# Performance work log

Hardware: AMD Instinct MI355X
Metric: run time of the kernel (lower is better)

The kernel has to match this reference:

```python
import jax, jax.numpy as jnp
import numpy as np

B, S, D = 4, 2048, 1024
H, K = 16, 64
EPS = 1e-3  # Keras LayerNormalization default epsilon


def setup_inputs() -> dict:
    key = jax.random.key(0)
    ks = jax.random.split(key, 11)
    s = 0.02
    return {
        "x":  jax.random.normal(ks[0], (B, S, D), jnp.float32),
        "Wq": jax.random.normal(ks[1], (D, H, K), jnp.float32) * s,
        "bq": jnp.zeros((H, K), jnp.float32),
        "Wk": jax.random.normal(ks[2], (D, H, K), jnp.float32) * s,
        "bk": jnp.zeros((H, K), jnp.float32),
        "Wv": jax.random.normal(ks[3], (D, H, K), jnp.float32) * s,
        "bv": jnp.zeros((H, K), jnp.float32),
        "Wo": jax.random.normal(ks[4], (H, K, D), jnp.float32) * s,
        "bo": jnp.zeros((D,), jnp.float32),
        "gamma": jnp.ones((D,), jnp.float32),
        "beta":  jnp.zeros((D,), jnp.float32),
    }


def reference(x, Wq, bq, Wk, bk, Wv, bv, Wo, bo, gamma, beta):
    # QKV projections (Keras MHA einsum form): [B,S,D] -> [B,S,H,K]
    q = jnp.einsum("bsd,dhk->bshk", x, Wq) + bq
    k = jnp.einsum("bsd,dhk->bshk", x, Wk) + bk
    v = jnp.einsum("bsd,dhk->bshk", x, Wv) + bv
    scale = 1.0 / jnp.sqrt(jnp.asarray(K, x.dtype))
    scores = jnp.einsum("bqhk,bshk->bhqs", q, k) * scale  # [B,H,S,S]
    attn = jax.nn.softmax(scores, axis=-1)
    ctx = jnp.einsum("bhqs,bshk->bqhk", attn, v)           # [B,S,H,K]
    attn_out = jnp.einsum("bqhk,hkd->bqd", ctx, Wo) + bo   # [B,S,D]
    # residual + LayerNorm (over last axis)
    y = x + attn_out
    mu = jnp.mean(y, axis=-1, keepdims=True)
    var = jnp.mean(jnp.square(y - mu), axis=-1, keepdims=True)
    return (y - mu) * jax.lax.rsqrt(var + EPS) * gamma + beta
```

## Files before the change

### kernel.cpp

```cpp
#include <hip/hip_runtime.h>

typedef float f32x4 __attribute__((ext_vector_type(4)));
typedef float f32x16 __attribute__((ext_vector_type(16)));
typedef __bf16 bf16x8 __attribute__((ext_vector_type(8)));
typedef __bf16 bf16x4 __attribute__((ext_vector_type(4)));
typedef __bf16 bf16x2 __attribute__((ext_vector_type(2)));
typedef unsigned short us4 __attribute__((ext_vector_type(4)));

#define DEV __device__ __forceinline__

DEV unsigned short f2bf(float f) {
  union { float f; unsigned int u; } v; v.f = f;
  unsigned int u = v.u;
  return (unsigned short)((u + 0x7FFFu + ((u >> 16) & 1u)) >> 16);
}

typedef const __attribute__((address_space(1))) void* gvp;
typedef __attribute__((address_space(3))) void* lvp;

DEV void gll16(const void* g, void* l) {
  __builtin_amdgcn_global_load_lds((gvp)g, (lvp)l, 16, 0, 0);
}

DEV float fexp2(float x) { return __builtin_amdgcn_exp2f(x); }

DEV void plswap(unsigned& a, unsigned& b) {
  asm("v_permlane32_swap_b32 %0, %1" : "+v"(a), "+v"(b));
}
DEV float xhalf_sum(float v) {
  union { float f; unsigned u; } a, b;
  a.f = v; b.f = v;
  plswap(a.u, b.u);
  return a.f + b.f;
}

__global__ void k_convert(const float* __restrict__ in, unsigned short* __restrict__ out, int n4) {
  int i = blockIdx.x * blockDim.x + threadIdx.x;
  if (i < n4) {
    float4 v = ((const float4*)in)[i];
    us4 o = { f2bf(v.x), f2bf(v.y), f2bf(v.z), f2bf(v.w) };
    ((us4*)out)[i] = o;
  }
}

__global__ void k_transpose4(const float* __restrict__ w0, const float* __restrict__ w1,
                             const float* __restrict__ w2, const float* __restrict__ w3,
                             unsigned short* __restrict__ o0, unsigned short* __restrict__ o1,
                             unsigned short* __restrict__ o2, unsigned short* __restrict__ o3) {
  const float* in = (blockIdx.z == 0) ? w0 : (blockIdx.z == 1) ? w1 : (blockIdx.z == 2) ? w2 : w3;
  unsigned short* out = (blockIdx.z == 0) ? o0 : (blockIdx.z == 1) ? o1 : (blockIdx.z == 2) ? o2 : o3;
  __shared__ float tile[32][33];
  const int bx = blockIdx.x * 32, by = blockIdx.y * 32;
  const int tx = threadIdx.x, ty = threadIdx.y;
#pragma unroll
  for (int r = 0; r < 4; ++r)
    tile[ty + r * 8][tx] = in[(size_t)(by + ty + r * 8) * 1024 + bx + tx];
  __syncthreads();
#pragma unroll
  for (int r = 0; r < 4; ++r)
    out[(size_t)(bx + ty + r * 8) * 1024 + by + tx] = f2bf(tile[tx][ty + r * 8]);
}

__global__ void k_gemm_qkv(const unsigned short* __restrict__ xb,
                           const unsigned short* __restrict__ wqt,
                           const unsigned short* __restrict__ wkt,
                           const unsigned short* __restrict__ wvt,
                           const float* __restrict__ bq, const float* __restrict__ bk,
                           const float* __restrict__ bv,
                           unsigned short* __restrict__ qb, unsigned short* __restrict__ kb,
                           unsigned short* __restrict__ vtb) {
  __shared__ unsigned short SM[2][128 * 64];
  unsigned short* As = SM[0];
  unsigned short* Bs = SM[1];
  const int tid = threadIdx.x;
  const int lane = tid & 63;
  const int wave = tid >> 6;
  const int l15 = lane & 15;
  const int lq  = lane >> 4;
  const int wm = wave >> 1, wn = wave & 1;
  const int z = blockIdx.z;

  const unsigned short* A;
  const unsigned short* Bt;
  int mbase, nbase;
  if (z == 2) { A = wvt; Bt = xb; mbase = blockIdx.y * 128; nbase = blockIdx.x * 128; }
  else        { A = xb; Bt = z ? wkt : wqt; mbase = blockIdx.x * 128; nbase = blockIdx.y * 128; }

  f32x4 acc[4][4] = {};

  for (int kt = 0; kt < 1024; kt += 64) {
    __syncthreads();
#pragma unroll
    for (int c = 0; c < 4; ++c) {
      int e = (c * 256 + tid) * 8;
      int row = e >> 6;
      int o2 = (e * 2) ^ ((row & 7) << 4);
      int col = (o2 >> 1) & 63;
      gll16(A + (size_t)(mbase + row) * 1024 + kt + col,
            As + (c * 256 + (tid & ~63)) * 8);
      gll16(Bt + (size_t)(nbase + row) * 1024 + kt + col,
            Bs + (c * 256 + (tid & ~63)) * 8);
    }
    __syncthreads();
#pragma unroll
    for (int ks = 0; ks < 2; ++ks) {
      bf16x8 af[4], bfv[4];
#pragma unroll
      for (int i = 0; i < 4; ++i) {
        int row = wm * 64 + i * 16 + l15;
        int off = row * 128 + ((((ks << 2) | lq) ^ (row & 7)) << 4);
        af[i] = *(const bf16x8*)((const char*)As + off);
      }
#pragma unroll
      for (int j = 0; j < 4; ++j) {
        int row = wn * 64 + j * 16 + l15;
        int off = row * 128 + ((((ks << 2) | lq) ^ (row & 7)) << 4);
        bfv[j] = *(const bf16x8*)((const char*)Bs + off);
      }
#pragma unroll
      for (int i = 0; i < 4; ++i)
#pragma unroll
        for (int j = 0; j < 4; ++j)
          acc[i][j] = __builtin_amdgcn_mfma_f32_16x16x32_bf16(bfv[j], af[i], acc[i][j], 0, 0, 0);
    }
  }

  const float scale = (z == 0) ? 0.18033688011112042f : 1.0f;
  const float* bias = (z == 0) ? bq : (z == 1) ? bk : bv;
  unsigned short* outp = (z == 0) ? qb : (z == 1) ? kb : vtb;

  float4 bj[4];
  if (z < 2) {
#pragma unroll
    for (int j = 0; j < 4; ++j)
      bj[j] = *(const float4*)&bias[nbase + wn * 64 + j * 16 + lq * 4];
  }

  __syncthreads();
  char* T = (char*)SM;
#pragma unroll
  for (int i = 0; i < 4; ++i) {
    const int miL = wm * 64 + i * 16 + l15;
    const int sw = (miL & 7) << 4;
    const float bm = (z == 2) ? bias[mbase + miL] : 0.f;
#pragma unroll
    for (int j = 0; j < 4; ++j) {
      const int nj2 = (wn * 64 + j * 16 + lq * 4) * 2;
      bf16x4 p;
#pragma unroll
      for (int r = 0; r < 4; ++r) {
        float v = acc[i][j][r];
        v = (z < 2) ? (v + ((const float*)&bj[j])[r]) * scale : (v + bm);
        p[r] = (__bf16)v;
      }
      *(bf16x4*)(T + miL * 256 + (nj2 ^ sw)) = p;
    }
  }
  __syncthreads();

#pragma unroll
  for (int c = 0; c < 8; ++c) {
    const int lin = c * 256 + tid;
    const int row = lin >> 4;
    const int s16 = lin & 15;
    bf16x8 vv = *(const bf16x8*)(T + row * 256 + ((s16 * 16) ^ ((row & 7) << 4)));
    const int mi = mbase + row;
    const int nj = nbase + s16 * 8;
    size_t gaddr;
    if (z < 2) {
      gaddr = (((size_t)((mi >> 11) * 16 + (nj >> 6)) * 2048 + (mi & 2047)) << 6) + (nj & 63);
    } else {
      gaddr = ((size_t)(((nj >> 11) * 16 + (mi >> 6)) * 64 + (mi & 63))) * 2048 + (nj & 2047);
    }
    *(bf16x8*)(outp + gaddr) = vv;
  }
}

__global__ void k_gemm_out(const unsigned short* __restrict__ A,
                           const unsigned short* __restrict__ Bt,
                           const float* __restrict__ bias,
                           float* __restrict__ outp,
                           const float* __restrict__ xres) {
  __shared__ unsigned short As[128 * 64];
  __shared__ unsigned short Bs[128 * 64];
  const int tid = threadIdx.x;
  const int lane = tid & 63;
  const int wave = tid >> 6;
  const int l15 = lane & 15;
  const int lq  = lane >> 4;
  const int wm = wave >> 1, wn = wave & 1;
  const int mbase = blockIdx.x * 128;
  const int nbase = blockIdx.y * 128;

  f32x4 acc[4][4] = {};

  for (int kt = 0; kt < 1024; kt += 64) {
    __syncthreads();
#pragma unroll
    for (int c = 0; c < 4; ++c) {
      int e = (c * 256 + tid) * 8;
      int row = e >> 6;
      int o2 = (e * 2) ^ ((row & 7) << 4);
      int col = (o2 >> 1) & 63;
      gll16(A + (size_t)(mbase + row) * 1024 + kt + col,
            As + (c * 256 + (tid & ~63)) * 8);
      gll16(Bt + (size_t)(nbase + row) * 1024 + kt + col,
            Bs + (c * 256 + (tid & ~63)) * 8);
    }
    __syncthreads();
#pragma unroll
    for (int ks = 0; ks < 2; ++ks) {
      bf16x8 af[4], bfv[4];
#pragma unroll
      for (int i = 0; i < 4; ++i) {
        int row = wm * 64 + i * 16 + l15;
        int off = row * 128 + ((((ks << 2) | lq) ^ (row & 7)) << 4);
        af[i] = *(const bf16x8*)((const char*)As + off);
      }
#pragma unroll
      for (int j = 0; j < 4; ++j) {
        int row = wn * 64 + j * 16 + l15;
        int off = row * 128 + ((((ks << 2) | lq) ^ (row & 7)) << 4);
        bfv[j] = *(const bf16x8*)((const char*)Bs + off);
      }
#pragma unroll
      for (int i = 0; i < 4; ++i)
#pragma unroll
        for (int j = 0; j < 4; ++j)
          acc[i][j] = __builtin_amdgcn_mfma_f32_16x16x32_bf16(af[i], bfv[j], acc[i][j], 0, 0, 0);
    }
  }

#pragma unroll
  for (int i = 0; i < 4; ++i)
#pragma unroll
    for (int j = 0; j < 4; ++j)
#pragma unroll
      for (int r = 0; r < 4; ++r) {
        int mi = mbase + wm * 64 + i * 16 + lq * 4 + r;
        int nj = nbase + wn * 64 + j * 16 + l15;
        size_t idx = (size_t)mi * 1024 + nj;
        outp[idx] = acc[i][j][r] + bias[nj] + xres[idx];
      }
}

__global__ __launch_bounds__(256, 4) void k_attn(const unsigned short* __restrict__ q,
                       const unsigned short* __restrict__ k,
                       const unsigned short* __restrict__ vt,
                       unsigned short* __restrict__ ctx) {
  __shared__ unsigned short KV[2][2][64 * 64];

  const int tid = threadIdx.x;
  const int lane = tid & 63;
  const int wave = tid >> 6;
  const int l31 = lane & 31;
  const int l5 = lane >> 5;

  const int bid = blockIdx.x;
  const int swz = (bid & 7) * 128 + (bid >> 3);
  const int bh = swz >> 4;
  const int qtile = swz & 15;
  const int qbase = qtile * 128;
  const size_t sl = (size_t)bh << 17;

  const int qrow = qbase + wave * 32 + l31;
  bf16x8 qreg[4];
#pragma unroll
  for (int ds = 0; ds < 4; ++ds)
    qreg[ds] = *(const bf16x8*)(q + sl + (size_t)qrow * 64 + ds * 16 + l5 * 8);

#define STAGE_KV(BUF, TT) do {                                                 \
    const int kvb_ = (TT) * 64;                                                \
    _Pragma("unroll")                                                          \
    for (int c = 0; c < 2; ++c) {                                              \
      int e = (c * 256 + tid) * 8;                                             \
      int row_ = e >> 6;                                                       \
      int o2 = (e * 2) ^ ((row_ & 7) << 4);                                    \
      int col_ = (o2 >> 1) & 63;                                               \
      gll16(k + sl + (size_t)(kvb_ + row_) * 64 + col_,                        \
            KV[BUF][0] + (c * 256 + (tid & ~63)) * 8);                         \
      gll16(vt + sl + (size_t)row_ * 2048 + kvb_ + col_,                       \
            KV[BUF][1] + (c * 256 + (tid & ~63)) * 8);                         \
    }                                                                          \
  } while (0)

  STAGE_KV(0, 0);
  __syncthreads();

  f32x16 acc0 = {}, acc1 = {};
  float lrow = 0.f;

  for (int t = 0; t < 32; ++t) {
    const int cur = t & 1;
    if (t < 31) STAGE_KV(cur ^ 1, t + 1);

    const char* Ksc = (const char*)KV[cur][0];
    const char* Vtc = (const char*)KV[cur][1];

    bf16x8 kf0[4], kf1[4];
#pragma unroll
    for (int ds = 0; ds < 4; ++ds) {
      int r0 = l31, r1 = 32 + l31;
      kf0[ds] = *(const bf16x8*)(Ksc + r0 * 128 + ((ds * 32 + l5 * 16) ^ ((r0 & 7) << 4)));
      kf1[ds] = *(const bf16x8*)(Ksc + r1 * 128 + ((ds * 32 + l5 * 16) ^ ((r1 & 7) << 4)));
    }
    f32x16 s0 = {}, s1 = {};
    __builtin_amdgcn_s_setprio(1);
#pragma unroll
    for (int ds = 0; ds < 4; ++ds)
      s0 = __builtin_amdgcn_mfma_f32_32x32x16_bf16(kf0[ds], qreg[ds], s0, 0, 0, 0);
#pragma unroll
    for (int ds = 0; ds < 4; ++ds)
      s1 = __builtin_amdgcn_mfma_f32_32x32x16_bf16(kf1[ds], qreg[ds], s1, 0, 0, 0);
    __builtin_amdgcn_s_setprio(0);
    __builtin_amdgcn_sched_barrier(0);

    unsigned pk0[8], pk1[8];
    float r0s = 0.f, r1s = 0.f, r2s = 0.f, r3s = 0.f;
#pragma unroll
    for (int m = 0; m < 8; ++m) {
      float a0 = fexp2(s0[2 * m]), a1 = fexp2(s0[2 * m + 1]);
      float b0 = fexp2(s1[2 * m]), b1 = fexp2(s1[2 * m + 1]);
      r0s += a0; r1s += a1; r2s += b0; r3s += b1;
      union { bf16x2 v; unsigned u; } ua, ub;
      ua.v = bf16x2{ (__bf16)a0, (__bf16)a1 };
      ub.v = bf16x2{ (__bf16)b0, (__bf16)b1 };
      pk0[m] = ua.u; pk1[m] = ub.u;
    }
    lrow += (r0s + r1s) + (r2s + r3s);
    __builtin_amdgcn_sched_barrier(0);

    bf16x8 av0[4], av1[4];
#pragma unroll
    for (int kvg = 0; kvg < 4; ++kvg) {
      int r0 = l31, r1 = 32 + l31;
      av0[kvg] = *(const bf16x8*)(Vtc + r0 * 128 + ((kvg * 32 + l5 * 16) ^ ((r0 & 7) << 4)));
      av1[kvg] = *(const bf16x8*)(Vtc + r1 * 128 + ((kvg * 32 + l5 * 16) ^ ((r1 & 7) << 4)));
    }
#pragma unroll
    for (int kvh = 0; kvh < 2; ++kvh) {
      unsigned* pk = kvh ? pk1 : pk0;
#pragma unroll
      for (int g = 0; g < 2; ++g) {
        unsigned a0_ = pk[4 * g],     b0_ = pk[4 * g + 2];
        unsigned a1_ = pk[4 * g + 1], b1_ = pk[4 * g + 3];
        plswap(a0_, b0_);
        plswap(a1_, b1_);
        union { unsigned u[4]; bf16x8 v; } pf;
        pf.u[0] = a0_; pf.u[1] = a1_; pf.u[2] = b0_; pf.u[3] = b1_;
        const int kvg = 2 * kvh + g;
        __builtin_amdgcn_s_setprio(1);
        acc0 = __builtin_amdgcn_mfma_f32_32x32x16_bf16(av0[kvg], pf.v, acc0, 0, 0, 0);
        acc1 = __builtin_amdgcn_mfma_f32_32x32x16_bf16(av1[kvg], pf.v, acc1, 0, 0, 0);
        __builtin_amdgcn_s_setprio(0);
      }
    }

    __syncthreads();
  }

  const float inv = 1.f / xhalf_sum(lrow);

  unsigned short* TR = (unsigned short*)KV;
  const int qloc = wave * 32 + l31;
  const int swq = (qloc & 7) << 4;
#pragma unroll
  for (int dh = 0; dh < 2; ++dh) {
    const f32x16& ac = dh ? acc1 : acc0;
#pragma unroll
    for (int g3 = 0; g3 < 4; ++g3) {
      bf16x4 o4 = { (__bf16)(ac[4 * g3] * inv), (__bf16)(ac[4 * g3 + 1] * inv),
                    (__bf16)(ac[4 * g3 + 2] * inv), (__bf16)(ac[4 * g3 + 3] * inv) };
      *(bf16x4*)((char*)TR + qloc * 128 + ((dh * 64 + g3 * 16 + l5 * 8) ^ swq)) = o4;
    }
  }
  __syncthreads();

  const int b = bh >> 4, h = bh & 15;
  {
    int row = tid >> 1, half = tid & 1;
    int sw = (row & 7) << 4;
    unsigned short* gdst = ctx + (size_t)(b * 2048 + qbase + row) * 1024 + h * 64 + half * 32;
#pragma unroll
    for (int i = 0; i < 4; ++i) {
      bf16x8 vv = *(const bf16x8*)((const char*)TR + row * 128 + ((half * 64 + i * 16) ^ sw));
      *(bf16x8*)(gdst + i * 8) = vv;
    }
  }
#undef STAGE_KV
}

__global__ void k_ln(const float* __restrict__ y, const float* __restrict__ gamma,
                     const float* __restrict__ beta, float* __restrict__ out) {
  const int row = blockIdx.x;
  const int tid = threadIdx.x;
  const float4 v = ((const float4*)(y + (size_t)row * 1024))[tid];
  float sum = v.x + v.y + v.z + v.w;
  float sq = v.x * v.x + v.y * v.y + v.z * v.z + v.w * v.w;
#pragma unroll
  for (int m = 1; m <= 32; m <<= 1) {
    sum += __shfl_xor(sum, m);
    sq  += __shfl_xor(sq, m);
  }
  __shared__ float s1[4], s2[4];
  const int wv = tid >> 6, lane = tid & 63;
  if (lane == 0) { s1[wv] = sum; s2[wv] = sq; }
  __syncthreads();
  sum = s1[0] + s1[1] + s1[2] + s1[3];
  sq  = s2[0] + s2[1] + s2[2] + s2[3];
  const float mu = sum * (1.f / 1024.f);
  const float rs = rsqrtf(sq * (1.f / 1024.f) - mu * mu + 1e-3f);
  const float4 g  = ((const float4*)gamma)[tid];
  const float4 bb = ((const float4*)beta)[tid];
  float4 o;
  o.x = (v.x - mu) * rs * g.x + bb.x;
  o.y = (v.y - mu) * rs * g.y + bb.y;
  o.z = (v.z - mu) * rs * g.z + bb.z;
  o.w = (v.w - mu) * rs * g.w + bb.w;
  ((float4*)(out + (size_t)row * 1024))[tid] = o;
}

extern "C" void kernel_launch(void* const* d_in, const int* in_sizes, int n_in,
                              void* d_out, int out_size, void* d_ws, size_t ws_size,
                              hipStream_t stream) {
  const float* x  = (const float*)d_in[0];
  const float* Wq = (const float*)d_in[1];
  const float* bq = (const float*)d_in[2];
  const float* Wk = (const float*)d_in[3];
  const float* bk = (const float*)d_in[4];
  const float* Wv = (const float*)d_in[5];
  const float* bv = (const float*)d_in[6];
  const float* Wo = (const float*)d_in[7];
  const float* bo = (const float*)d_in[8];
  const float* gamma = (const float*)d_in[9];
  const float* beta  = (const float*)d_in[10];
  float* out = (float*)d_out;

  char* ws = (char*)d_ws;
  const size_t MB = 1024 * 1024;
  unsigned short* xb  = (unsigned short*)(ws);
  unsigned short* wqt = (unsigned short*)(ws + 16 * MB);
  unsigned short* wkt = (unsigned short*)(ws + 18 * MB);
  unsigned short* wvt = (unsigned short*)(ws + 20 * MB);
  unsigned short* wot = (unsigned short*)(ws + 22 * MB);
  unsigned short* qb  = (unsigned short*)(ws + 24 * MB);
  unsigned short* kb  = (unsigned short*)(ws + 40 * MB);
  unsigned short* vtb = (unsigned short*)(ws + 56 * MB);
  unsigned short* ctx = (unsigned short*)(ws + 72 * MB);
  float* yb = (float*)(ws + 24 * MB);

  k_convert<<<8192, 256, 0, stream>>>(x, xb, 2097152);
  dim3 tb(32, 8), tg(32, 32, 4);
  k_transpose4<<<tg, tb, 0, stream>>>(Wq, Wk, Wv, Wo, wqt, wkt, wvt, wot);

  k_gemm_qkv<<<dim3(64, 8, 3), 256, 0, stream>>>(xb, wqt, wkt, wvt, bq, bk, bv, qb, kb, vtb);

  k_attn<<<1024, 256, 0, stream>>>(qb, kb, vtb, ctx);

  k_gemm_out<<<dim3(64, 8), 256, 0, stream>>>(ctx, wot, bo, yb, x);

  k_ln<<<8192, 256, 0, stream>>>(yb, gamma, beta, out);
  (void)in_sizes; (void)n_in; (void)out_size; (void)ws_size;
}
```

Before: 183.3 us.

## Merge prep kernels, bf16 residual path, new attention LDS swizzle

Combines the x conversion and the weight transposes into one launch to save a kernel launch. The output GEMM now writes a bf16 y through an LDS-staged, coalesced epilogue and reads the residual from the bf16 copy of x. LayerNorm reads bf16 input, which halves the y traffic but lowers precision of the residual and pre-norm values. The attention kernel gets a new K/V LDS swizzle and widens its setprio region around the PV MFMAs.

```diff
diff --git a/kernel.cpp b/kernel.cpp
--- a/kernel.cpp
+++ b/kernel.cpp
@@ -34,24 +34,28 @@
   return a.f + b.f;
 }
 
-__global__ void k_convert(const float* __restrict__ in, unsigned short* __restrict__ out, int n4) {
-  int i = blockIdx.x * blockDim.x + threadIdx.x;
-  if (i < n4) {
-    float4 v = ((const float4*)in)[i];
+__global__ void k_pre(const float* __restrict__ x, unsigned short* __restrict__ xb,
+                      const float* __restrict__ w0, const float* __restrict__ w1,
+                      const float* __restrict__ w2, const float* __restrict__ w3,
+                      unsigned short* __restrict__ o0, unsigned short* __restrict__ o1,
+                      unsigned short* __restrict__ o2, unsigned short* __restrict__ o3) {
+  __shared__ float tile[32][33];
+  const int bid = blockIdx.x;
+  const int tid = threadIdx.x;
+  if (bid < 8192) {
+    int i = bid * 256 + tid;
+    float4 v = ((const float4*)x)[i];
     us4 o = { f2bf(v.x), f2bf(v.y), f2bf(v.z), f2bf(v.w) };
-    ((us4*)out)[i] = o;
-  }
-}
-
-__global__ void k_transpose4(const float* __restrict__ w0, const float* __restrict__ w1,
-                             const float* __restrict__ w2, const float* __restrict__ w3,
-                             unsigned short* __restrict__ o0, unsigned short* __restrict__ o1,
-                             unsigned short* __restrict__ o2, unsigned short* __restrict__ o3) {
-  const float* in = (blockIdx.z == 0) ? w0 : (blockIdx.z == 1) ? w1 : (blockIdx.z == 2) ? w2 : w3;
-  unsigned short* out = (blockIdx.z == 0) ? o0 : (blockIdx.z == 1) ? o1 : (blockIdx.z == 2) ? o2 : o3;
-  __shared__ float tile[32][33];
-  const int bx = blockIdx.x * 32, by = blockIdx.y * 32;
-  const int tx = threadIdx.x, ty = threadIdx.y;
+    ((us4*)xb)[i] = o;
+    return;
+  }
+  int t = bid - 8192;
+  const int z = t >> 10;
+  t &= 1023;
+  const float* in = (z == 0) ? w0 : (z == 1) ? w1 : (z == 2) ? w2 : w3;
+  unsigned short* out = (z == 0) ? o0 : (z == 1) ? o1 : (z == 2) ? o2 : o3;
+  const int bx = (t & 31) * 32, by = (t >> 5) * 32;
+  const int tx = tid & 31, ty = tid >> 5;
 #pragma unroll
   for (int r = 0; r < 4; ++r)
     tile[ty + r * 8][tx] = in[(size_t)(by + ty + r * 8) * 1024 + bx + tx];
@@ -179,10 +183,11 @@
 __global__ void k_gemm_out(const unsigned short* __restrict__ A,
                            const unsigned short* __restrict__ Bt,
                            const float* __restrict__ bias,
-                           float* __restrict__ outp,
-                           const float* __restrict__ xres) {
-  __shared__ unsigned short As[128 * 64];
-  __shared__ unsigned short Bs[128 * 64];
+                           unsigned short* __restrict__ yb,
+                           const unsigned short* __restrict__ xres) {
+  __shared__ unsigned short SM[2][128 * 64];
+  unsigned short* As = SM[0];
+  unsigned short* Bs = SM[1];
   const int tid = threadIdx.x;
   const int lane = tid & 63;
   const int wave = tid >> 6;
@@ -227,21 +232,47 @@
       for (int i = 0; i < 4; ++i)
 #pragma unroll
         for (int j = 0; j < 4; ++j)
-          acc[i][j] = __builtin_amdgcn_mfma_f32_16x16x32_bf16(af[i], bfv[j], acc[i][j], 0, 0, 0);
-    }
-  }
-
-#pragma unroll
-  for (int i = 0; i < 4; ++i)
-#pragma unroll
-    for (int j = 0; j < 4; ++j)
-#pragma unroll
-      for (int r = 0; r < 4; ++r) {
-        int mi = mbase + wm * 64 + i * 16 + lq * 4 + r;
-        int nj = nbase + wn * 64 + j * 16 + l15;
-        size_t idx = (size_t)mi * 1024 + nj;
-        outp[idx] = acc[i][j][r] + bias[nj] + xres[idx];
-      }
+          acc[i][j] = __builtin_amdgcn_mfma_f32_16x16x32_bf16(bfv[j], af[i], acc[i][j], 0, 0, 0);
+    }
+  }
+
+  float4 bj[4];
+#pragma unroll
+  for (int j = 0; j < 4; ++j)
+    bj[j] = *(const float4*)&bias[nbase + wn * 64 + j * 16 + lq * 4];
+
+  __syncthreads();
+  char* T = (char*)SM;
+#pragma unroll
+  for (int i = 0; i < 4; ++i) {
+    const int miL = wm * 64 + i * 16 + l15;
+    const int sw = (miL & 7) << 4;
+#pragma unroll
+    for (int j = 0; j < 4; ++j) {
+      const int nj2 = (wn * 64 + j * 16 + lq * 4) * 2;
+      bf16x4 p;
+#pragma unroll
+      for (int r = 0; r < 4; ++r)
+        p[r] = (__bf16)(acc[i][j][r] + ((const float*)&bj[j])[r]);
+      *(bf16x4*)(T + miL * 256 + (nj2 ^ sw)) = p;
+    }
+  }
+  __syncthreads();
+
+#pragma unroll
+  for (int c = 0; c < 8; ++c) {
+    const int lin = c * 256 + tid;
+    const int row = lin >> 4;
+    const int s16 = lin & 15;
+    bf16x8 vv = *(const bf16x8*)(T + row * 256 + ((s16 * 16) ^ ((row & 7) << 4)));
+    const size_t g = (size_t)(mbase + row) * 1024 + nbase + s16 * 8;
+    bf16x8 xv = *(const bf16x8*)(xres + g);
+    bf16x8 ov;
+#pragma unroll
+    for (int e = 0; e < 8; ++e)
+      ov[e] = (__bf16)((float)vv[e] + (float)xv[e]);
+    *(bf16x8*)(yb + g) = ov;
+  }
 }
 
 __global__ __launch_bounds__(256, 4) void k_attn(const unsigned short* __restrict__ q,
@@ -255,6 +286,8 @@
   const int wave = tid >> 6;
   const int l31 = lane & 31;
   const int l5 = lane >> 5;
+  const int prl = l31 >> 1;
+  const int b3  = (l31 & 1) << 3;
 
   const int bid = blockIdx.x;
   const int swz = (bid & 7) * 128 + (bid >> 3);
@@ -273,13 +306,14 @@
     const int kvb_ = (TT) * 64;                                                \
     _Pragma("unroll")                                                          \
     for (int c = 0; c < 2; ++c) {                                              \
-      int e = (c * 256 + tid) * 8;                                             \
-      int row_ = e >> 6;                                                       \
-      int o2 = (e * 2) ^ ((row_ & 7) << 4);                                    \
-      int col_ = (o2 >> 1) & 63;                                               \
-      gll16(k + sl + (size_t)(kvb_ + row_) * 64 + col_,                        \
+      int ci = c * 256 + tid;                                                  \
+      int pr_ = ci >> 4;                                                       \
+      int u_ = (ci & 15) ^ (pr_ & 15);                                         \
+      int lrow_ = pr_ * 2 + (u_ >> 3);                                         \
+      int lc_ = u_ & 7;                                                        \
+      gll16(k + sl + (size_t)(kvb_ + lrow_) * 64 + lc_ * 8,                    \
             KV[BUF][0] + (c * 256 + (tid & ~63)) * 8);                         \
-      gll16(vt + sl + (size_t)row_ * 2048 + kvb_ + col_,                       \
+      gll16(vt + sl + (size_t)lrow_ * 2048 + kvb_ + lc_ * 8,                   \
             KV[BUF][1] + (c * 256 + (tid & ~63)) * 8);                         \
     }                                                                          \
   } while (0)
@@ -300,9 +334,9 @@
     bf16x8 kf0[4], kf1[4];
 #pragma unroll
     for (int ds = 0; ds < 4; ++ds) {
-      int r0 = l31, r1 = 32 + l31;
-      kf0[ds] = *(const bf16x8*)(Ksc + r0 * 128 + ((ds * 32 + l5 * 16) ^ ((r0 & 7) << 4)));
-      kf1[ds] = *(const bf16x8*)(Ksc + r1 * 128 + ((ds * 32 + l5 * 16) ^ ((r1 & 7) << 4)));
+      int sc = (b3 | (2 * ds + l5)) ^ prl;
+      kf0[ds] = *(const bf16x8*)(Ksc + prl * 256 + sc * 16);
+      kf1[ds] = *(const bf16x8*)(Ksc + 4096 + prl * 256 + sc * 16);
     }
     f32x16 s0 = {}, s1 = {};
     __builtin_amdgcn_s_setprio(1);
@@ -333,10 +367,11 @@
     bf16x8 av0[4], av1[4];
 #pragma unroll
     for (int kvg = 0; kvg < 4; ++kvg) {
-      int r0 = l31, r1 = 32 + l31;
-      av0[kvg] = *(const bf16x8*)(Vtc + r0 * 128 + ((kvg * 32 + l5 * 16) ^ ((r0 & 7) << 4)));
-      av1[kvg] = *(const bf16x8*)(Vtc + r1 * 128 + ((kvg * 32 + l5 * 16) ^ ((r1 & 7) << 4)));
-    }
+      int sc = (b3 | (2 * kvg + l5)) ^ prl;
+      av0[kvg] = *(const bf16x8*)(Vtc + prl * 256 + sc * 16);
+      av1[kvg] = *(const bf16x8*)(Vtc + 4096 + prl * 256 + sc * 16);
+    }
+    __builtin_amdgcn_s_setprio(1);
 #pragma unroll
     for (int kvh = 0; kvh < 2; ++kvh) {
       unsigned* pk = kvh ? pk1 : pk0;
@@ -349,12 +384,11 @@
         union { unsigned u[4]; bf16x8 v; } pf;
         pf.u[0] = a0_; pf.u[1] = a1_; pf.u[2] = b0_; pf.u[3] = b1_;
         const int kvg = 2 * kvh + g;
-        __builtin_amdgcn_s_setprio(1);
         acc0 = __builtin_amdgcn_mfma_f32_32x32x16_bf16(av0[kvg], pf.v, acc0, 0, 0, 0);
         acc1 = __builtin_amdgcn_mfma_f32_32x32x16_bf16(av1[kvg], pf.v, acc1, 0, 0, 0);
-        __builtin_amdgcn_s_setprio(0);
-      }
-    }
+      }
+    }
+    __builtin_amdgcn_s_setprio(0);
 
     __syncthreads();
   }
@@ -390,13 +424,14 @@
 #undef STAGE_KV
 }
 
-__global__ void k_ln(const float* __restrict__ y, const float* __restrict__ gamma,
+__global__ void k_ln(const unsigned short* __restrict__ y, const float* __restrict__ gamma,
                      const float* __restrict__ beta, float* __restrict__ out) {
   const int row = blockIdx.x;
   const int tid = threadIdx.x;
-  const float4 v = ((const float4*)(y + (size_t)row * 1024))[tid];
-  float sum = v.x + v.y + v.z + v.w;
-  float sq = v.x * v.x + v.y * v.y + v.z * v.z + v.w * v.w;
+  const bf16x4 v4 = *(const bf16x4*)(y + (size_t)row * 1024 + tid * 4);
+  float v0 = (float)v4[0], v1 = (float)v4[1], v2 = (float)v4[2], v3 = (float)v4[3];
+  float sum = v0 + v1 + v2 + v3;
+  float sq = v0 * v0 + v1 * v1 + v2 * v2 + v3 * v3;
 #pragma unroll
   for (int m = 1; m <= 32; m <<= 1) {
     sum += __shfl_xor(sum, m);
@@ -413,10 +448,10 @@
   const float4 g  = ((const float4*)gamma)[tid];
   const float4 bb = ((const float4*)beta)[tid];
   float4 o;
-  o.x = (v.x - mu) * rs * g.x + bb.x;
-  o.y = (v.y - mu) * rs * g.y + bb.y;
-  o.z = (v.z - mu) * rs * g.z + bb.z;
-  o.w = (v.w - mu) * rs * g.w + bb.w;
+  o.x = (v0 - mu) * rs * g.x + bb.x;
+  o.y = (v1 - mu) * rs * g.y + bb.y;
+  o.z = (v2 - mu) * rs * g.z + bb.z;
+  o.w = (v3 - mu) * rs * g.w + bb.w;
   ((float4*)(out + (size_t)row * 1024))[tid] = o;
 }
 
@@ -447,17 +482,15 @@
   unsigned short* kb  = (unsigned short*)(ws + 40 * MB);
   unsigned short* vtb = (unsigned short*)(ws + 56 * MB);
   unsigned short* ctx = (unsigned short*)(ws + 72 * MB);
-  float* yb = (float*)(ws + 24 * MB);
-
-  k_convert<<<8192, 256, 0, stream>>>(x, xb, 2097152);
-  dim3 tb(32, 8), tg(32, 32, 4);
-  k_transpose4<<<tg, tb, 0, stream>>>(Wq, Wk, Wv, Wo, wqt, wkt, wvt, wot);
+  unsigned short* yb  = (unsigned short*)(ws + 24 * MB);
+
+  k_pre<<<12288, 256, 0, stream>>>(x, xb, Wq, Wk, Wv, Wo, wqt, wkt, wvt, wot);
 
   k_gemm_qkv<<<dim3(64, 8, 3), 256, 0, stream>>>(xb, wqt, wkt, wvt, bq, bk, bv, qb, kb, vtb);
 
   k_attn<<<1024, 256, 0, stream>>>(qb, kb, vtb, ctx);
 
-  k_gemm_out<<<dim3(64, 8), 256, 0, stream>>>(ctx, wot, bo, yb, x);
+  k_gemm_out<<<dim3(64, 8), 256, 0, stream>>>(ctx, wot, bo, yb, xb);
 
   k_ln<<<8192, 256, 0, stream>>>(yb, gamma, beta, out);
   (void)in_sizes; (void)n_in; (void)out_size; (void)ws_size;
```

New measurement: 175.2 us. 4.4% less time.
